# Performance work log

Measured on AMD Instinct MI355X. Metric: run time of the kernel, lower is better.

The kernel has to match this reference:

```python
import jax, jax.numpy as jnp
import numpy as np

ZC, ZS = 32, 16
NS = [16384, 4096, 1024, 256, 64]  # mesh node counts per level
K_CH = 6
DEG = 12

def _key(i):
    return jax.random.fold_in(jax.random.key(0), i)

def setup_inputs():
    d = {}
    d["x"] = jax.random.normal(_key(0), (2, 16, NS[0], 3), jnp.float32)
    enc_dims = [(6, 16), (16, 16), (16, 16), (16, 32)]
    dec_dims = [(32, 16), (16, 16), (16, 16), (16, 3)]
    i = 1
    for p, dims in (("enc", enc_dims), ("decc", dec_dims), ("decs", dec_dims)):
        for l, (fi, fo) in enumerate(dims):
            d[p + "_W" + str(l)] = 0.1 * jax.random.normal(_key(i), (K_CH, fi, fo), jnp.float32); i += 1
            if p == "enc" or l < 3:  # last decoder convs have bias=None
                d[p + "_b" + str(l)] = jnp.zeros((fo,), jnp.float32)
    nfz = NS[4] * 32  # _n_features_before_z
    d["mu_W"] = 0.1 * jax.random.normal(_key(i), (ZC + ZS, nfz), jnp.float32); i += 1
    d["mu_b"] = jnp.zeros((ZC + ZS,), jnp.float32)
    d["linc_W"] = 0.1 * jax.random.normal(_key(i), (nfz, ZC), jnp.float32); i += 1
    d["linc_b"] = jnp.zeros((nfz,), jnp.float32)
    d["lins_W"] = 0.1 * jax.random.normal(_key(i), (nfz, ZC + 2 * ZS), jnp.float32); i += 1
    d["lins_b"] = jnp.zeros((nfz,), jnp.float32)
    for l in range(4):
        d["ei" + str(l)] = jax.random.randint(_key(i), (2, DEG * NS[l]), 0, NS[l], jnp.int32); i += 1
    d["ei4"] = jax.random.randint(_key(i), (2, DEG * NS[0]), 0, NS[0], jnp.int32); i += 1
    for l in range(4):
        d["ds_i" + str(l)] = jax.random.randint(_key(i), (NS[l + 1], 3), 0, NS[l], jnp.int32); i += 1
        d["ds_w" + str(l)] = jax.random.uniform(_key(i), (NS[l + 1], 3), jnp.float32); i += 1
        d["us_i" + str(l)] = jax.random.randint(_key(i), (NS[l], 3), 0, NS[l + 1], jnp.int32); i += 1
        d["us_w" + str(l)] = jax.random.uniform(_key(i), (NS[l], 3), jnp.float32); i += 1
    return d

def _norm(ei, n):
    # ChebConv_Coma.norm: D^-1/2 A D^-1/2 edge weights (unit edge weights)
    row, col = ei[0], ei[1]
    deg = jnp.zeros((n,), jnp.float32).at[row].add(1.0)
    dis = jnp.where(deg > 0, 1.0 / jnp.sqrt(jnp.maximum(deg, 1.0)), 0.0)
    return dis[row] * dis[col]

def _prop(x, ei, w, n):
    # sparse matvec: out[:, dst] += w_e * x[:, src]   (x: [B, n, F])
    msg = x[:, ei[0], :] * w[None, :, None]
    return jnp.zeros((x.shape[0], n, x.shape[2]), x.dtype).at[:, ei[1], :].add(msg)

def _cheb(x, ei, w, Wk, b, n):
    # Chebyshev recurrence: T0=x, T1=Lx, Tk=2L T_{k-1} - T_{k-2}
    out = jnp.einsum('bnf,fg->bng', x, Wk[0])
    Tx0 = x
    Tx1 = _prop(x, ei, w, n)
    out = out + jnp.einsum('bnf,fg->bng', Tx1, Wk[1])
    for k in range(2, Wk.shape[0]):
        Tx2 = 2.0 * _prop(Tx1, ei, w, n) - Tx0
        out = out + jnp.einsum('bnf,fg->bng', Tx2, Wk[k])
        Tx0, Tx1 = Tx1, Tx2
    return out if b is None else out + b

def _pool(x, idx, w):
    # sparse pooling matrix, 3 nnz/row: out[:, i] = sum_k w[i,k] * x[:, idx[i,k]]
    return jnp.einsum('bnkf,nk->bnf', x[:, idx, :], w)

def _phase(x):
    # PhaseTensor: doubles last dim with cos/sin phase modulation over time axis 1
    T = x.shape[1]
    th = 2.0 * jnp.pi * jnp.arange(T, dtype=x.dtype) / T
    shp = (1, T) + (1,) * (x.ndim - 2)
    return jnp.concatenate([x * jnp.cos(th).reshape(shp), x * jnp.sin(th).reshape(shp)], axis=-1)

def _model(FL, IL):
    (x, eW0, eb0, eW1, eb1, eW2, eb2, eW3, eb3,
     cW0, cb0, cW1, cb1, cW2, cb2, cW3,
     sW0, sb0, sW1, sb1, sW2, sb2, sW3,
     mu_W, mu_b, linc_W, linc_b, lins_W, lins_b,
     ds_w0, ds_w1, ds_w2, ds_w3, us_w0, us_w1, us_w2, us_w3) = FL
    (ei0, ei1, ei2, ei3, ei4,
     ds_i0, ds_i1, ds_i2, ds_i3, us_i0, us_i1, us_i2, us_i3) = IL
    eis = [ei0, ei1, ei2, ei3, ei4]
    lvl_n = [NS[0], NS[1], NS[2], NS[3], NS[0]]
    nrm = [_norm(eis[l], lvl_n[l]) for l in range(5)]
    B, T, N0, F0 = x.shape
    # phase_input: [B,T,N,3] -> [B,T,N,6]; fold time into batch for the conv stack
    h = _phase(x).reshape(B * T, N0, 2 * F0)
    encW = [(eW0, eb0), (eW1, eb1), (eW2, eb2), (eW3, eb3)]
    dsl = [(ds_i0, ds_w0), (ds_i1, ds_w1), (ds_i2, ds_w2), (ds_i3, ds_w3)]
    usl = [(us_i0, us_w0), (us_i1, us_w1), (us_i2, us_w2), (us_i3, us_w3)]
    for l in range(4):
        h = jax.nn.relu(_cheb(h, eis[l], nrm[l], encW[l][0], encW[l][1], NS[l]))
        h = _pool(h, dsl[l][0], dsl[l][1])
    h = h.reshape(B, T, -1)  # [B, T, N4*32]
    mu = jnp.einsum('btf,zf->btz', h, mu_W) + mu_b
    # faithful to torch code: per-t cat along dim 0 (time-major) then reshape(-1, T, z)
    mu_c = jnp.mean(jnp.swapaxes(mu[..., :ZC], 0, 1).reshape(B, T, ZC), axis=1)
    mu_s = jnp.mean(jnp.swapaxes(mu[..., ZC:], 0, 1).reshape(B, T, ZS), axis=1)

    def dec(z, Ws, bs, lW, lb, relu_first):
        y = z @ lW.T + lb
        if relu_first:
            y = jax.nn.relu(y)
        y = y.reshape(y.shape[0], NS[4], Ws[0].shape[1])  # [*, N4, 32]
        for i in range(3):  # n_layers - 1 upsample+conv+relu
            lvl = 3 - i
            y = _pool(y, usl[lvl][0], usl[lvl][1])
            y = jax.nn.relu(_cheb(y, eis[lvl], nrm[lvl], Ws[i], bs[i], NS[lvl]))
        y = _pool(y, usl[0][0], usl[0][1])
        return _cheb(y, eis[4], nrm[4], Ws[3], None, NS[0])  # final conv, no bias/relu

    s_avg = dec(mu_c, [cW0, cW1, cW2, cW3], [cb0, cb1, cb2], linc_W, linc_b, False)
    # decoder_s, vectorized over timeframes by folding T into batch
    zs_ph = _phase(jnp.broadcast_to(mu_s[:, None, :], (B, T, ZS)))  # [B,T,2*ZS]
    zc_rep = jnp.broadcast_to(mu_c[:, None, :], (B, T, ZC))
    zin = jnp.concatenate([zc_rep, zs_ph], axis=-1).reshape(B * T, ZC + 2 * ZS)
    ds_t = dec(zin, [sW0, sW1, sW2, sW3], [sb0, sb1, sb2], lins_W, lins_b, True).reshape(B, T, N0, 3)
    s_t = s_avg[:, None] + ds_t
    return mu_c, mu_s, s_avg, s_t

def reference(x, enc_W0, enc_b0, enc_W1, enc_b1, enc_W2, enc_b2, enc_W3, enc_b3, decc_W0, decc_b0, decc_W1, decc_b1, decc_W2, decc_b2, decc_W3, decs_W0, decs_b0, decs_W1, decs_b1, decs_W2, decs_b2, decs_W3, mu_W, mu_b, linc_W, linc_b, lins_W, lins_b, ds_w0, ds_w1, ds_w2, ds_w3, us_w0, us_w1, us_w2, us_w3, ei0, ei1, ei2, ei3, ei4, ds_i0, ds_i1, ds_i2, ds_i3, us_i0, us_i1, us_i2, us_i3):
    FL = (x, enc_W0, enc_b0, enc_W1, enc_b1, enc_W2, enc_b2, enc_W3, enc_b3,
          decc_W0, decc_b0, decc_W1, decc_b1, decc_W2, decc_b2, decc_W3,
          decs_W0, decs_b0, decs_W1, decs_b1, decs_W2, decs_b2, decs_W3,
          mu_W, mu_b, linc_W, linc_b, lins_W, lins_b,
          ds_w0, ds_w1, ds_w2, ds_w3, us_w0, us_w1, us_w2, us_w3)
    IL = (ei0, ei1, ei2, ei3, ei4, ds_i0, ds_i1, ds_i2, ds_i3, us_i0, us_i1, us_i2, us_i3)
    return _model(FL, IL)
```

## Files before the change

kernel.cpp:

```cpp
#include <hip/hip_runtime.h>
#include <cstdint>
#include <cstddef>

#define TPB 256

typedef float f32x4 __attribute__((ext_vector_type(4)));
typedef float f32x2 __attribute__((ext_vector_type(2)));
typedef int   i32x4 __attribute__((ext_vector_type(4)));

static inline int cdiv(long long a, int b){ return (int)((a + (long long)b - 1) / b); }

#define NTOT 38144
#define ETOT 457728
#define CTOT 762880
#define RPTOT 38149


template<int W>
__device__ __forceinline__ void vload(const float* __restrict__ p, float* r){
  if constexpr (W == 8){ vload<4>(p, r); vload<4>(p+4, r+4); }
  else if constexpr (W == 4){ f32x4 v = *reinterpret_cast<const f32x4*>(p); r[0]=v.x;r[1]=v.y;r[2]=v.z;r[3]=v.w; }
  else { f32x2 v = *reinterpret_cast<const f32x2*>(p); r[0]=v.x;r[1]=v.y; }
}
template<int W>
__device__ __forceinline__ void vstore(float* __restrict__ p, const float* r){
  if constexpr (W == 8){ vstore<4>(p, r); vstore<4>(p+4, r+4); }
  else if constexpr (W == 4){ f32x4 v; v.x=r[0];v.y=r[1];v.z=r[2];v.w=r[3]; *reinterpret_cast<f32x4*>(p) = v; }
  else { f32x2 v; v.x=r[0];v.y=r[1]; *reinterpret_cast<f32x2*>(p) = v; }
}

template<int F>
__device__ __forceinline__ void loadrow(const float* __restrict__ p, float* r){
  #pragma unroll
  for (int q = 0; q < F/4; ++q) vload<4>(p + 4*q, r + 4*q);
}
template<int F>
__device__ __forceinline__ void storerow(float* __restrict__ p, const float* r){
  #pragma unroll
  for (int q = 0; q < F/4; ++q) vstore<4>(p + 4*q, r + 4*q);
}


__device__ __forceinline__ bool lvl_edge(int t, const int* e0,const int* e1,const int* e2,const int* e3,const int* e4,
                                         const int*& ei, int& E, int& noff, int& rpoff, int& rel){
  if (t < 196608){ ei=e0; E=196608; noff=0;     rpoff=0;     rel=t;        return true; }
  if (t < 245760){ ei=e1; E=49152;  noff=16384; rpoff=16385; rel=t-196608; return true; }
  if (t < 258048){ ei=e2; E=12288;  noff=20480; rpoff=20482; rel=t-245760; return true; }
  if (t < 261120){ ei=e3; E=3072;   noff=21504; rpoff=21507; rel=t-258048; return true; }
  if (t < 457728){ ei=e4; E=196608; noff=21760; rpoff=21764; rel=t-261120; return true; }
  return false;
}

__global__ void k_degs_all(const int* e0,const int* e1,const int* e2,const int* e3,const int* e4,
                           int* __restrict__ rowdeg, int* __restrict__ dstdeg){
  int t = blockIdx.x*blockDim.x + threadIdx.x;
  const int* ei; int E, noff, rpoff, rel;
  if (!lvl_edge(t, e0,e1,e2,e3,e4, ei,E,noff,rpoff,rel)) return;
  atomicAdd(&rowdeg[noff + ei[rel]], 1);
  atomicAdd(&dstdeg[noff + ei[E + rel]], 1);
}

__global__ void k_dis_all(const int* __restrict__ rowdeg, float* __restrict__ dis){
  int t = blockIdx.x*blockDim.x + threadIdx.x;
  if (t >= NTOT) return;
  int d = rowdeg[t];
  dis[t] = d > 0 ? rsqrtf((float)d) : 0.f;
}

__global__ void k_scan5(const int* __restrict__ dstdeg, int* __restrict__ rp, int* __restrict__ cursor){
  const int NnA[5]  = {16384,4096,1024,256,16384};
  const int NOFF[5] = {0,16384,20480,21504,21760};
  const int COFF[5] = {0,327680,409600,430080,435200};
  __shared__ int part[257];
  int l = blockIdx.x;
  int N = NnA[l];
  const int* cnt = dstdeg + NOFF[l];
  int* rpl = rp + NOFF[l] + l;
  int* cul = cursor + NOFF[l] + l;
  int tid = threadIdx.x;
  int chunk = (N + 255) / 256;
  int lo = tid*chunk; if (lo > N) lo = N;
  int hi = lo + chunk; if (hi > N) hi = N;
  int s = 0;
  for (int i = lo; i < hi; ++i) s += (cnt[i] + 7) & ~7;
  part[tid+1] = s;
  if (tid == 0) part[0] = COFF[l];
  __syncthreads();
  if (tid == 0){ for (int i = 1; i <= 256; ++i) part[i] += part[i-1]; }
  __syncthreads();
  int run = part[tid];
  for (int i = lo; i < hi; ++i){ rpl[i] = run; cul[i] = run; run += (cnt[i] + 7) & ~7; }
  if (tid == 0) rpl[N] = part[256];
}

__global__ void k_fill_all(const int* e0,const int* e1,const int* e2,const int* e3,const int* e4,
                           const float* __restrict__ dis, int* __restrict__ cursor,
                           int* __restrict__ srcs, float* __restrict__ w){
  int t = blockIdx.x*blockDim.x + threadIdx.x;
  const int* ei; int E, noff, rpoff, rel;
  if (!lvl_edge(t, e0,e1,e2,e3,e4, ei,E,noff,rpoff,rel)) return;
  int src = ei[rel], dst = ei[E + rel];
  int pos = atomicAdd(&cursor[rpoff + dst], 1);
  srcs[pos] = src;
  w[pos] = dis[noff + src] * dis[noff + dst];
}

__global__ void k_pad_all(const int* __restrict__ dstdeg, const int* __restrict__ rp,
                          int* __restrict__ srcs, float* __restrict__ w){
  int t = blockIdx.x*blockDim.x + threadIdx.x;
  if (t >= NTOT) return;
  int rpoff, n;
  if      (t < 16384){ rpoff = 0;     n = t; }
  else if (t < 20480){ rpoff = 16385; n = t - 16384; }
  else if (t < 21504){ rpoff = 20482; n = t - 20480; }
  else if (t < 21760){ rpoff = 21507; n = t - 21504; }
  else               { rpoff = 21764; n = t - 21760; }
  int j0 = rp[rpoff + n];
  int j1 = rp[rpoff + n + 1];
  int cnt = dstdeg[t];
  int sfill = cnt > 0 ? srcs[j0] : 0;
  for (int j = j0 + cnt; j < j1; ++j){ srcs[j] = sfill; w[j] = 0.f; }
}


template<int FinPad>
__device__ __forceinline__ void tmap(int N, int& gb, int& n, int& gs, int& sub, int& laneoff){
  constexpr int LPR = FinPad/4;
  gb = blockIdx.x & 7;
  int I = (blockIdx.x >> 3)*256 + threadIdx.x;
  n = I / FinPad;
  int u = I - n*FinPad;
  gs = u / LPR;
  sub = u - gs*LPR;
  laneoff = gs*FinPad + sub*4;
}

template<int FinPad>
__device__ __forceinline__ void gather8_t(const float* __restrict__ base,
                                          const int* __restrict__ srcs, const float* __restrict__ w,
                                          int j0, int j1, int laneoff, float* acc){
  constexpr int RS = 4*FinPad;
  #pragma unroll
  for (int q = 0; q < 4; ++q) acc[q] = 0.f;
  for (int j = j0; j < j1; j += 8){
    i32x4 sa = *reinterpret_cast<const i32x4*>(srcs + j);
    i32x4 sb = *reinterpret_cast<const i32x4*>(srcs + j + 4);
    f32x4 wa = *reinterpret_cast<const f32x4*>(w + j);
    f32x4 wb = *reinterpret_cast<const f32x4*>(w + j + 4);
    float v0[4], v1[4], v2[4], v3[4], v4[4], v5[4], v6[4], v7[4];
    vload<4>(base + (size_t)sa.x*RS + laneoff, v0);
    vload<4>(base + (size_t)sa.y*RS + laneoff, v1);
    vload<4>(base + (size_t)sa.z*RS + laneoff, v2);
    vload<4>(base + (size_t)sa.w*RS + laneoff, v3);
    vload<4>(base + (size_t)sb.x*RS + laneoff, v4);
    vload<4>(base + (size_t)sb.y*RS + laneoff, v5);
    vload<4>(base + (size_t)sb.z*RS + laneoff, v6);
    vload<4>(base + (size_t)sb.w*RS + laneoff, v7);
    #pragma unroll
    for (int q = 0; q < 4; ++q){
      acc[q] = fmaf(wa.x, v0[q], acc[q]);
      acc[q] = fmaf(wa.y, v1[q], acc[q]);
      acc[q] = fmaf(wa.z, v2[q], acc[q]);
      acc[q] = fmaf(wa.w, v3[q], acc[q]);
      acc[q] = fmaf(wb.x, v4[q], acc[q]);
      acc[q] = fmaf(wb.y, v5[q], acc[q]);
      acc[q] = fmaf(wb.z, v6[q], acc[q]);
      acc[q] = fmaf(wb.w, v7[q], acc[q]);
    }
  }
}

template<int FinPad, int FinReal, int Fout>
__device__ __forceinline__ void gemm_t(const float* ts, const float* __restrict__ Wk,
                                       int sub, float* o){
  constexpr int LPR = FinPad/4;
  int lane = (int)threadIdx.x & 63;
  int lanebase = lane & ~(LPR-1);
  float tv[FinPad];
  #pragma unroll
  for (int s = 0; s < LPR; ++s)
    #pragma unroll
    for (int q = 0; q < 4; ++q)
      tv[s*4+q] = __shfl(ts[q], lanebase + s, 64);
  if constexpr (Fout % 4 == 0){
    constexpr int OPL = Fout/LPR;
    #pragma unroll
    for (int fi = 0; fi < FinReal; ++fi)
      #pragma unroll
      for (int q = 0; q < OPL; ++q)
        o[q] = fmaf(tv[fi], Wk[fi*Fout + sub*OPL + q], o[q]);
  } else {
    if (sub < Fout){
      #pragma unroll
      for (int fi = 0; fi < FinReal; ++fi)
        o[0] = fmaf(tv[fi], Wk[fi*Fout + sub], o[0]);
    }
  }
}

template<int FinPad, int PRE>
__global__ void k_pre_t(const float* __restrict__ psrc, const int* __restrict__ pidx,
                        const float* __restrict__ pw, float* __restrict__ bufX,
                        int N, int Nin){
  int gb, n, gs, sub, laneoff;
  tmap<FinPad>(N, gb, n, gs, sub, laneoff);
  constexpr int RS = 4*FinPad;
  float r[4];
  if constexpr (PRE == 1){
    int g = (gb<<2) | gs;
    int t = g & 15;
    float th = 6.283185307179586f * (float)t / 16.0f;
    float sn, cs; sincosf(th, &sn, &cs);
    const float* xr = psrc + ((size_t)g*16384 + n)*3;
    #pragma unroll
    for (int q = 0; q < 4; ++q){
      int f = sub*4 + q;
      float v = 0.f;
      if (f < 6) v = xr[f % 3] * (f < 3 ? cs : sn);
      r[q] = v;
    }
  } else {
    int i0 = pidx[n*3+0], i1 = pidx[n*3+1], i2 = pidx[n*3+2];
    float w0 = pw[n*3+0], w1 = pw[n*3+1], w2 = pw[n*3+2];
    const float* pb = psrc + (size_t)gb*Nin*RS + laneoff;
    float a[4], b[4], c[4];
    vload<4>(pb + (size_t)i0*RS, a);
    vload<4>(pb + (size_t)i1*RS, b);
    vload<4>(pb + (size_t)i2*RS, c);
    #pragma unroll
    for (int q = 0; q < 4; ++q) r[q] = fmaf(w0, a[q], fmaf(w1, b[q], w2*c[q]));
  }
  vstore<4>(bufX + (size_t)gb*N*RS + (size_t)n*RS + laneoff, r);
}

template<int FinPad, int FinReal, int Fout>
__global__ void k_first_t(const int* __restrict__ rp, const int* __restrict__ srcs, const float* __restrict__ w,
                          const float* __restrict__ bufX, float* __restrict__ bufT1, float* __restrict__ out,
                          const float* __restrict__ W6, const float* __restrict__ bias, int N){
  constexpr int LPR = FinPad/4;
  constexpr int OPL = (Fout % 4 == 0) ? Fout/LPR : 1;
  constexpr int RS = 4*FinPad;
  int gb, n, gs, sub, laneoff;
  tmap<FinPad>(N, gb, n, gs, sub, laneoff);
  const float* gbase = bufX + (size_t)gb*N*RS;
  float t0[4]; vload<4>(gbase + (size_t)n*RS + laneoff, t0);
  float t1[4];
  gather8_t<FinPad>(gbase, srcs, w, rp[n], rp[n+1], laneoff, t1);
  vstore<4>(bufT1 + (size_t)gb*N*RS + (size_t)n*RS + laneoff, t1);
  float o[OPL];
  if constexpr (Fout % 4 == 0){
    #pragma unroll
    for (int q = 0; q < OPL; ++q) o[q] = bias ? bias[sub*OPL + q] : 0.f;
  } else {
    o[0] = (bias && sub < Fout) ? bias[sub] : 0.f;
  }
  gemm_t<FinPad,FinReal,Fout>(t0, W6, sub, o);
  gemm_t<FinPad,FinReal,Fout>(t1, W6 + (size_t)FinReal*Fout, sub, o);
  if constexpr (Fout % 4 == 0){
    vstore<OPL>(out + ((size_t)(gb*N + n)*4 + gs)*Fout + sub*OPL, o);
  } else {
    if (sub < Fout){
      int g = (gb<<2)|gs;
      out[((size_t)g*N + n)*3 + sub] = o[0];
    }
  }
}

template<int FinPad, int FinReal, int Fout>
__global__ void k_step_t(const int* __restrict__ rp, const int* __restrict__ srcs, const float* __restrict__ w,
                         const float* __restrict__ Tm1, float* __restrict__ P, float* __restrict__ out,
                         const float* __restrict__ Wk, const float* __restrict__ savg,
                         int N, int relu, int last){
  constexpr int LPR = FinPad/4;
  constexpr int OPL = (Fout % 4 == 0) ? Fout/LPR : 1;
  constexpr int RS = 4*FinPad;
  int gb, n, gs, sub, laneoff;
  tmap<FinPad>(N, gb, n, gs, sub, laneoff);
  const float* gbase = Tm1 + (size_t)gb*N*RS;
  float tk[4];
  gather8_t<FinPad>(gbase, srcs, w, rp[n], rp[n+1], laneoff, tk);
  float tm2[4]; vload<4>(P + (size_t)gb*N*RS + (size_t)n*RS + laneoff, tm2);
  #pragma unroll
  for (int q = 0; q < 4; ++q) tk[q] = 2.f*tk[q] - tm2[q];
  if (!last) vstore<4>(P + (size_t)gb*N*RS + (size_t)n*RS + laneoff, tk);
  float o[OPL];
  if constexpr (Fout % 4 == 0){
    vload<OPL>(out + ((size_t)(gb*N + n)*4 + gs)*Fout + sub*OPL, o);
  } else {
    o[0] = 0.f;
    if (sub < Fout) o[0] = out[((size_t)((gb<<2)|gs)*N + n)*3 + sub];
  }
  gemm_t<FinPad,FinReal,Fout>(tk, Wk, sub, o);
  if constexpr (Fout % 4 == 0){
    if (last && relu){
      #pragma unroll
      for (int q = 0; q < OPL; ++q) o[q] = fmaxf(o[q], 0.f);
    }
    vstore<OPL>(out + ((size_t)(gb*N + n)*4 + gs)*Fout + sub*OPL, o);
  } else {
    if (sub < Fout){
      float v = o[0];
      if (last && relu) v = fmaxf(v, 0.f);
      int g = (gb<<2)|gs;
      if (last && savg) v += savg[((size_t)(g>>4)*N + n)*3 + sub];
      out[((size_t)g*N + n)*3 + sub] = v;
    }
  }
}


template<int FPL, int FinPad>
__device__ __forceinline__ void gather8(const float* __restrict__ gb,
                                        const int* __restrict__ srcs, const float* __restrict__ w,
                                        int j0, int j1, int sub, float* acc){
  #pragma unroll
  for (int q = 0; q < FPL; ++q) acc[q] = 0.f;
  for (int j = j0; j < j1; j += 8){
    i32x4 sa = *reinterpret_cast<const i32x4*>(srcs + j);
    i32x4 sb = *reinterpret_cast<const i32x4*>(srcs + j + 4);
    f32x4 wa = *reinterpret_cast<const f32x4*>(w + j);
    f32x4 wb = *reinterpret_cast<const f32x4*>(w + j + 4);
    float v0[FPL], v1[FPL], v2[FPL], v3[FPL], v4[FPL], v5[FPL], v6[FPL], v7[FPL];
    vload<FPL>(gb + (size_t)sa.x*FinPad + sub*FPL, v0);
    vload<FPL>(gb + (size_t)sa.y*FinPad + sub*FPL, v1);
    vload<FPL>(gb + (size_t)sa.z*FinPad + sub*FPL, v2);
    vload<FPL>(gb + (size_t)sa.w*FinPad + sub*FPL, v3);
    vload<FPL>(gb + (size_t)sb.x*FinPad + sub*FPL, v4);
    vload<FPL>(gb + (size_t)sb.y*FinPad + sub*FPL, v5);
    vload<FPL>(gb + (size_t)sb.z*FinPad + sub*FPL, v6);
    vload<FPL>(gb + (size_t)sb.w*FinPad + sub*FPL, v7);
    #pragma unroll
    for (int q = 0; q < FPL; ++q){
      acc[q] = fmaf(wa.x, v0[q], acc[q]);
      acc[q] = fmaf(wa.y, v1[q], acc[q]);
      acc[q] = fmaf(wa.z, v2[q], acc[q]);
      acc[q] = fmaf(wa.w, v3[q], acc[q]);
      acc[q] = fmaf(wb.x, v4[q], acc[q]);
      acc[q] = fmaf(wb.y, v5[q], acc[q]);
      acc[q] = fmaf(wb.z, v6[q], acc[q]);
      acc[q] = fmaf(wb.w, v7[q], acc[q]);
    }
  }
}

template<int FinPad, int FinReal, int Fout>
__device__ __forceinline__ void gemm_acc(const float* ts, const float* __restrict__ Wk,
                                         int sub, int lanebase, float* o){
  constexpr int FPL = FinPad/4;
  float tv[FinPad];
  #pragma unroll
  for (int s = 0; s < 4; ++s)
    #pragma unroll
    for (int q = 0; q < FPL; ++q)
      tv[s*FPL+q] = __shfl(ts[q], lanebase + s, 64);
  if constexpr (Fout % 4 == 0){
    constexpr int OPL = Fout/4;
    #pragma unroll
    for (int fi = 0; fi < FinReal; ++fi)
      #pragma unroll
      for (int q = 0; q < OPL; ++q)
        o[q] = fmaf(tv[fi], Wk[fi*Fout + sub*OPL + q], o[q]);
  } else {
    if (sub < Fout){
      #pragma unroll
      for (int fi = 0; fi < FinReal; ++fi)
        o[0] = fmaf(tv[fi], Wk[fi*Fout + sub], o[0]);
    }
  }
}

template<int FinPad>
__device__ __forceinline__ void pool_row(const float* __restrict__ psrc, const int* __restrict__ pidx,
                                         const float* __restrict__ pw, int n, int g, int Nin, int sub,
                                         float* r){
  constexpr int FPL = FinPad/4;
  int i0 = pidx[n*3+0], i1 = pidx[n*3+1], i2 = pidx[n*3+2];
  float w0 = pw[n*3+0], w1 = pw[n*3+1], w2 = pw[n*3+2];
  const float* bsrc = psrc + (size_t)g*Nin*FinPad + sub*FPL;
  float a[FPL], b[FPL], c[FPL];
  vload<FPL>(bsrc + (size_t)i0*FinPad, a);
  vload<FPL>(bsrc + (size_t)i1*FinPad, b);
  vload<FPL>(bsrc + (size_t)i2*FinPad, c);
  #pragma unroll
  for (int q = 0; q < FPL; ++q) r[q] = fmaf(w0, a[q], fmaf(w1, b[q], w2*c[q]));
}

template<int FinPad>
__global__ void k_pre_f(const float* __restrict__ psrc, const int* __restrict__ pidx,
                        const float* __restrict__ pw, float* __restrict__ bufX,
                        int G, int logN, int Nin){
  constexpr int FPL = FinPad/4;
  long long i4 = (long long)blockIdx.x*blockDim.x + threadIdx.x;
  if (i4 >= ((long long)G << logN)*4) return;
  int sub = (int)(i4 & 3);
  long long i = i4 >> 2;
  int N = 1 << logN;
  int n = (int)(i & (N-1));
  int g = (int)(i >> logN);
  float r[FPL];
  pool_row<FinPad>(psrc, pidx, pw, n, g, Nin, sub, r);
  vstore<FPL>(bufX + (size_t)i*FinPad + sub*FPL, r);
}

template<int FinPad, int FinReal, int Fout>
__global__ void k_first_f(const int* __restrict__ rp, const int* __restrict__ srcs, const float* __restrict__ w,
                          const float* __restrict__ bufX, float* __restrict__ bufT1, float* __restrict__ out,
                          const float* __restrict__ W6, const float* __restrict__ bias,
                          int G, int logN){
  constexpr int FPL = FinPad/4;
  constexpr int OPL = (Fout % 4 == 0) ? Fout/4 : 1;
  long long i4 = (long long)blockIdx.x*blockDim.x + threadIdx.x;
  if (i4 >= ((long long)G << logN)*4) return;
  int sub = (int)(i4 & 3);
  long long i = i4 >> 2;
  int N = 1 << logN;
  int n = (int)(i & (N-1));
  int lanebase = ((int)threadIdx.x & 63) & ~3;
  const float* gb = bufX + (size_t)(i - n)*FinPad;
  float t0[FPL]; vload<FPL>(bufX + (size_t)i*FinPad + sub*FPL, t0);
  float t1[FPL];
  gather8<FPL,FinPad>(gb, srcs, w, rp[n], rp[n+1], sub, t1);
  vstore<FPL>(bufT1 + (size_t)i*FinPad + sub*FPL, t1);
  float o[OPL];
  if constexpr (Fout % 4 == 0){
    #pragma unroll
    for (int q = 0; q < OPL; ++q) o[q] = bias ? bias[sub*OPL + q] : 0.f;
  } else {
    o[0] = (bias && sub < Fout) ? bias[sub] : 0.f;
  }
  gemm_acc<FinPad,FinReal,Fout>(t0, W6, sub, lanebase, o);
  gemm_acc<FinPad,FinReal,Fout>(t1, W6 + (size_t)FinReal*Fout, sub, lanebase, o);
  if constexpr (Fout % 4 == 0) vstore<OPL>(out + (size_t)i*Fout + sub*OPL, o);
  else if (sub < Fout) out[(size_t)i*Fout + sub] = o[0];
}

template<int FinPad, int FinReal, int Fout>
__global__ void k_step_f(const int* __restrict__ rp, const int* __restrict__ srcs, const float* __restrict__ w,
                         const float* __restrict__ Tm1, float* __restrict__ P, float* __restrict__ out,
                         const float* __restrict__ Wk, const float* __restrict__ savg,
                         int G, int logN, int relu, int last){
  constexpr int FPL = FinPad/4;
  constexpr int OPL = (Fout % 4 == 0) ? Fout/4 : 1;
  long long i4 = (long long)blockIdx.x*blockDim.x + threadIdx.x;
  if (i4 >= ((long long)G << logN)*4) return;
  int sub = (int)(i4 & 3);
  long long i = i4 >> 2;
  int N = 1 << logN;
  int n = (int)(i & (N-1));
  int lanebase = ((int)threadIdx.x & 63) & ~3;
  const float* gb = Tm1 + (size_t)(i - n)*FinPad;
  float tk[FPL];
  gather8<FPL,FinPad>(gb, srcs, w, rp[n], rp[n+1], sub, tk);
  float tm2[FPL]; vload<FPL>(P + (size_t)i*FinPad + sub*FPL, tm2);
  #pragma unroll
  for (int q = 0; q < FPL; ++q) tk[q] = 2.f*tk[q] - tm2[q];
  if (!last) vstore<FPL>(P + (size_t)i*FinPad + sub*FPL, tk);
  float o[OPL];
  if constexpr (Fout % 4 == 0) vload<OPL>(out + (size_t)i*Fout + sub*OPL, o);
  else { o[0] = (sub < Fout) ? out[(size_t)i*Fout + sub] : 0.f; }
  gemm_acc<FinPad,FinReal,Fout>(tk, Wk, sub, lanebase, o);
  if constexpr (Fout % 4 == 0){
    if (last && relu){
      #pragma unroll
      for (int q = 0; q < OPL; ++q) o[q] = fmaxf(o[q], 0.f);
    }
    vstore<OPL>(out + (size_t)i*Fout + sub*OPL, o);
  } else {
    if (sub < Fout){
      float v = o[0];
      if (last && relu) v = fmaxf(v, 0.f);
      if (last && savg){
        int g = (int)(i >> logN);
        v += savg[((size_t)(g>>4)*N + n)*3 + sub];
      }
      out[(size_t)i*Fout + sub] = v;
    }
  }
}


__global__ void k_mu_t(const float* __restrict__ h_t, const float* __restrict__ W,
                       const float* __restrict__ b, float* __restrict__ mu){
  int wid = (blockIdx.x*blockDim.x + threadIdx.x) >> 6;
  int lane = threadIdx.x & 63;
  if (wid >= 32*48) return;
  int z = wid % 48, g = wid / 48;
  const float* wr = W + (size_t)z*2048;
  const float* hb = h_t + (size_t)(g>>2)*64*128 + (g&3)*32;
  float acc = 0.f;
  for (int f2 = lane; f2 < 2048; f2 += 64)
    acc = fmaf(hb[(size_t)(f2>>5)*128 + (f2&31)], wr[f2], acc);
  for (int o = 32; o > 0; o >>= 1) acc += __shfl_down(acc, o, 64);
  if (lane == 0) mu[wid] = acc + b[z];
}

__global__ void k_mucs(const float* __restrict__ mu, float* __restrict__ muc,
                       float* __restrict__ mus, float* __restrict__ out){
  int i = blockIdx.x*blockDim.x + threadIdx.x;
  if (i >= 96) return;
  int z = i % 48, bp = i / 48;
  float acc = 0.f;
  for (int b = 0; b < 2; ++b)
    for (int t = 8*bp; t < 8*bp + 8; ++t)
      acc += mu[(b*16 + t)*48 + z];
  acc *= (1.f/16.f);
  if (z < 32){ muc[bp*32 + z] = acc; out[bp*32 + z] = acc; }
  else       { mus[bp*16 + (z-32)] = acc; out[64 + bp*16 + (z-32)] = acc; }
}

__global__ void k_zin(const float* __restrict__ muc, const float* __restrict__ mus,
                      float* __restrict__ zin){
  int i = blockIdx.x*blockDim.x + threadIdx.x;
  if (i >= 32*64) return;
  int c = i % 64, g = i / 64;
  int b = g / 16, t = g % 16;
  float v;
  if (c < 32){
    v = muc[b*32 + c];
  } else {
    float th = 6.283185307179586f * (float)t / 16.0f;
    int k = c - 32;
    int kk = (k < 16) ? k : (k - 16);
    float m = mus[b*16 + kk];
    v = (k < 16) ? m * cosf(th) : m * sinf(th);
  }
  zin[i] = v;
}

__global__ void k_lin(const float* __restrict__ z, const float* __restrict__ W,
                      const float* __restrict__ b, float* __restrict__ y,
                      int G, int Z, int relu){
  int i = blockIdx.x*blockDim.x + threadIdx.x;
  if (i >= G*2048) return;
  int f = i % 2048, g = i / 2048;
  const float* zr = z + (size_t)g*Z;
  const float* wr = W + (size_t)f*Z;
  float acc = b[f];
  for (int k = 0; k < Z; ++k) acc = fmaf(zr[k], wr[k], acc);
  if (relu) acc = fmaxf(acc, 0.f);
  y[i] = acc;
}

__global__ void k_lin_t(const float* __restrict__ z, const float* __restrict__ W,
                        const float* __restrict__ b, float* __restrict__ y_t,
                        int Z, int relu){
  int i = blockIdx.x*blockDim.x + threadIdx.x;
  if (i >= 32*2048) return;
  int f2 = i % 2048, g = i / 2048;
  const float* zr = z + (size_t)g*Z;
  const float* wr = W + (size_t)f2*Z;
  float acc = b[f2];
  for (int k = 0; k < Z; ++k) acc = fmaf(zr[k], wr[k], acc);
  if (relu) acc = fmaxf(acc, 0.f);
  y_t[(size_t)(g>>2)*64*128 + (size_t)(f2>>5)*128 + (g&3)*32 + (f2&31)] = acc;
}


struct LvlArgs {
  const int* rp; const int* srcs; const float* w;
  const float* psrc; const int* pidx; const float* pw;
  float* bufX; float* bufT1; float* out;
  const float* W6; const float* bias; const float* savg;
  int G; int logN; int Nin; int relu;
};

template<int FinPad, int FinReal, int Fout, int PRE>
static void run_level_t(hipStream_t s, const LvlArgs& a){
  int N = 1 << a.logN;
  int grid = 8 * (N*FinPad/256);
  k_pre_t<FinPad,PRE><<<grid,256,0,s>>>(a.psrc, a.pidx, a.pw, a.bufX, N, a.Nin);
  k_first_t<FinPad,FinReal,Fout><<<grid,256,0,s>>>(a.rp, a.srcs, a.w, a.bufX, a.bufT1, a.out,
                                                   a.W6, a.bias, N);
  float* Ab = a.bufT1; float* Bb = a.bufX;
  for (int k = 2; k <= 5; ++k){
    int last = (k == 5) ? 1 : 0;
    k_step_t<FinPad,FinReal,Fout><<<grid,256,0,s>>>(a.rp, a.srcs, a.w, Ab, Bb, a.out,
                                                    a.W6 + (size_t)k*FinReal*Fout,
                                                    last ? a.savg : nullptr,
                                                    N, a.relu, last);
    float* t = Ab; Ab = Bb; Bb = t;
  }
}

template<int FinPad, int FinReal, int Fout>
static void run_level_f(hipStream_t s, const LvlArgs& a){
  long long GN4 = ((long long)a.G << a.logN) * 4;
  int grid = cdiv(GN4, 256);
  k_pre_f<FinPad><<<grid,256,0,s>>>(a.psrc, a.pidx, a.pw, a.bufX, a.G, a.logN, a.Nin);
  k_first_f<FinPad,FinReal,Fout><<<grid,256,0,s>>>(a.rp, a.srcs, a.w, a.bufX, a.bufT1, a.out,
                                                   a.W6, a.bias, a.G, a.logN);
  float* Ab = a.bufT1; float* Bb = a.bufX;
  for (int k = 2; k <= 5; ++k){
    int last = (k == 5) ? 1 : 0;
    k_step_f<FinPad,FinReal,Fout><<<grid,256,0,s>>>(a.rp, a.srcs, a.w, Ab, Bb, a.out,
                                                    a.W6 + (size_t)k*FinReal*Fout,
                                                    last ? a.savg : nullptr,
                                                    a.G, a.logN, a.relu, last);
    float* t = Ab; Ab = Bb; Bb = t;
  }
}

extern "C" void kernel_launch(void* const* d_in, const int* in_sizes, int n_in,
                              void* d_out, int out_size, void* d_ws, size_t ws_size,
                              hipStream_t stream){
  const float* x = (const float*)d_in[0];
  const float* encW[4] = {(const float*)d_in[1],(const float*)d_in[3],(const float*)d_in[5],(const float*)d_in[7]};
  const float* encB[4] = {(const float*)d_in[2],(const float*)d_in[4],(const float*)d_in[6],(const float*)d_in[8]};
  const float* ccW[4]  = {(const float*)d_in[9],(const float*)d_in[11],(const float*)d_in[13],(const float*)d_in[15]};
  const float* ccB[3]  = {(const float*)d_in[10],(const float*)d_in[12],(const float*)d_in[14]};
  const float* csW[4]  = {(const float*)d_in[16],(const float*)d_in[18],(const float*)d_in[20],(const float*)d_in[22]};
  const float* csB[3]  = {(const float*)d_in[17],(const float*)d_in[19],(const float*)d_in[21]};
  const float* muW  = (const float*)d_in[23]; const float* muB  = (const float*)d_in[24];
  const float* lincW = (const float*)d_in[25]; const float* lincB = (const float*)d_in[26];
  const float* linsW = (const float*)d_in[27]; const float* linsB = (const float*)d_in[28];
  const int* ei[5] = {(const int*)d_in[29],(const int*)d_in[30],(const int*)d_in[31],
                      (const int*)d_in[32],(const int*)d_in[33]};
  const int* ds_i[4]; const float* ds_w[4]; const int* us_i[4]; const float* us_w[4];
  for (int l = 0; l < 4; ++l){
    ds_i[l] = (const int*)d_in[34 + 4*l]; ds_w[l] = (const float*)d_in[35 + 4*l];
    us_i[l] = (const int*)d_in[36 + 4*l]; us_w[l] = (const float*)d_in[37 + 4*l];
  }

  float* ws = (float*)d_ws;
  const size_t BIG = 8388608;
  float* B0 = ws + 0*BIG;
  float* B1 = ws + 1*BIG;
  float* B2 = ws + 2*BIG;
  float* B3 = ws + 3*BIG;
  size_t off = 4*BIG;

  int*   rp_all     = (int*)(ws + off); off += RPTOT;
  int*   cursor_all = (int*)(ws + off); off += RPTOT;
  off = (off + 3) & ~(size_t)3;
  int*   srcs_all   = (int*)(ws + off); off += CTOT;
  float* w_all      =        ws + off;  off += CTOT;
  int*   rowdeg     = (int*)(ws + off); off += NTOT;
  int*   dstdeg     = (int*)(ws + off); off += NTOT;
  float* dis        =        ws + off;  off += NTOT;
  float* hmu        =        ws + off;  off += (size_t)32*2048;
  float* mu         =        ws + off;  off += (size_t)32*48;
  float* muc        =        ws + off;  off += 64;
  float* mus        =        ws + off;  off += 32;
  float* zin        =        ws + off;  off += (size_t)32*64;

  float* outp = (float*)d_out;
  float* out_savg = outp + 96;
  float* out_st   = outp + 96 + 98304;

  hipMemsetAsync(rowdeg, 0, 2*(size_t)NTOT*sizeof(int), stream);
  k_degs_all<<<cdiv(ETOT,TPB),TPB,0,stream>>>(ei[0],ei[1],ei[2],ei[3],ei[4], rowdeg, dstdeg);
  k_dis_all<<<cdiv(NTOT,TPB),TPB,0,stream>>>(rowdeg, dis);
  k_scan5<<<5,256,0,stream>>>(dstdeg, rp_all, cursor_all);
  k_fill_all<<<cdiv(ETOT,TPB),TPB,0,stream>>>(ei[0],ei[1],ei[2],ei[3],ei[4], dis, cursor_all, srcs_all, w_all);
  k_pad_all<<<cdiv(NTOT,TPB),TPB,0,stream>>>(dstdeg, rp_all, srcs_all, w_all);

  const int RPOFF[5] = {0,16385,20482,21507,21764};
  const int* RP[5];
  for (int l = 0; l < 5; ++l) RP[l] = rp_all + RPOFF[l];

  run_level_t<8,6,16,1>(stream, {RP[0],srcs_all,w_all, x,nullptr,nullptr,
                                 B0,B1,B2, encW[0],encB[0],nullptr, 32,14,0,1});
  run_level_t<16,16,16,0>(stream, {RP[1],srcs_all,w_all, B2,ds_i[0],ds_w[0],
                                   B0,B1,B3, encW[1],encB[1],nullptr, 32,12,16384,1});
  run_level_t<16,16,16,0>(stream, {RP[2],srcs_all,w_all, B3,ds_i[1],ds_w[1],
                                   B0,B1,B2, encW[2],encB[2],nullptr, 32,10,4096,1});
  run_level_t<16,16,32,0>(stream, {RP[3],srcs_all,w_all, B2,ds_i[2],ds_w[2],
                                   B0,B1,B3, encW[3],encB[3],nullptr, 32,8,1024,1});
  {
    int grid = 8 * (64*32/256);
    k_pre_t<32,0><<<grid,256,0,stream>>>(B3, ds_i[3], ds_w[3], hmu, 64, 256);
  }

  k_mu_t<<<cdiv((long long)32*48*64,TPB),TPB,0,stream>>>(hmu, muW, muB, mu);
  k_mucs<<<1,128,0,stream>>>(mu, muc, mus, outp);

  k_lin<<<cdiv((long long)2*2048,TPB),TPB,0,stream>>>(muc, lincW, lincB, B2, 2, 32, 0);
  run_level_f<32,32,16>(stream, {RP[3],srcs_all,w_all, B2,us_i[3],us_w[3],
                                 B0,B1,B3, ccW[0],ccB[0],nullptr, 2,8,64,1});
  run_level_f<16,16,16>(stream, {RP[2],srcs_all,w_all, B3,us_i[2],us_w[2],
                                 B0,B1,B2, ccW[1],ccB[1],nullptr, 2,10,256,1});
  run_level_f<16,16,16>(stream, {RP[1],srcs_all,w_all, B2,us_i[1],us_w[1],
                                 B0,B1,B3, ccW[2],ccB[2],nullptr, 2,12,1024,1});
  run_level_f<16,16,3>(stream, {RP[4],srcs_all,w_all, B3,us_i[0],us_w[0],
                                B0,B1,out_savg, ccW[3],nullptr,nullptr, 2,14,4096,0});

  k_zin<<<cdiv(32*64,TPB),TPB,0,stream>>>(muc, mus, zin);
  k_lin_t<<<cdiv((long long)32*2048,TPB),TPB,0,stream>>>(zin, linsW, linsB, B2, 64, 1);
  run_level_t<32,32,16,0>(stream, {RP[3],srcs_all,w_all, B2,us_i[3],us_w[3],
                                   B0,B1,B3, csW[0],csB[0],nullptr, 32,8,64,1});
  run_level_t<16,16,16,0>(stream, {RP[2],srcs_all,w_all, B3,us_i[2],us_w[2],
                                   B0,B1,B2, csW[1],csB[1],nullptr, 32,10,256,1});
  run_level_t<16,16,16,0>(stream, {RP[1],srcs_all,w_all, B2,us_i[1],us_w[1],
                                   B0,B1,B3, csW[2],csB[2],nullptr, 32,12,1024,1});
  run_level_t<16,16,3,0>(stream, {RP[4],srcs_all,w_all, B3,us_i[0],us_w[0],
                                  B0,B1,out_st, csW[3],nullptr,out_savg, 32,14,4096,0});

  (void)in_sizes; (void)n_in; (void)out_size; (void)ws_size;
}
```

Measured before the change: 1.103 ms.

## Overlap content decoder and first pre-pass with main path on side stream

Creates a second non-blocking stream with events. The first-level input pre-pass runs concurrently with CSR graph construction, and the content decoder (2-graph batch) runs concurrently with the style decoder using separate scratch buffers D0-D3. The main stream waits on events only before the final style level, which needs out_savg. This targets the serialization of small, under-occupied kernels, at the cost of extra workspace and event synchronisation overhead.

```diff
diff --git a/kernel.cpp b/kernel.cpp
--- a/kernel.cpp
+++ b/kernel.cpp
@@ -14,6 +14,18 @@
 #define ETOT 457728
 #define CTOT 762880
 #define RPTOT 38149
+
+static hipStream_t g_s2 = nullptr;
+static hipEvent_t g_evF1 = nullptr, g_evPre = nullptr, g_evF2 = nullptr, g_evDecc = nullptr;
+__attribute__((constructor)) static void init_side_stream(){
+  if (hipStreamCreateWithFlags(&g_s2, hipStreamNonBlocking) != hipSuccess){ g_s2 = nullptr; return; }
+  if (hipEventCreateWithFlags(&g_evF1, hipEventDisableTiming) != hipSuccess ||
+      hipEventCreateWithFlags(&g_evPre, hipEventDisableTiming) != hipSuccess ||
+      hipEventCreateWithFlags(&g_evF2, hipEventDisableTiming) != hipSuccess ||
+      hipEventCreateWithFlags(&g_evDecc, hipEventDisableTiming) != hipSuccess){
+    g_s2 = nullptr;
+  }
+}
 
 
 template<int W>
@@ -370,22 +382,6 @@
 }
 
 template<int FinPad>
-__device__ __forceinline__ void pool_row(const float* __restrict__ psrc, const int* __restrict__ pidx,
-                                         const float* __restrict__ pw, int n, int g, int Nin, int sub,
-                                         float* r){
-  constexpr int FPL = FinPad/4;
-  int i0 = pidx[n*3+0], i1 = pidx[n*3+1], i2 = pidx[n*3+2];
-  float w0 = pw[n*3+0], w1 = pw[n*3+1], w2 = pw[n*3+2];
-  const float* bsrc = psrc + (size_t)g*Nin*FinPad + sub*FPL;
-  float a[FPL], b[FPL], c[FPL];
-  vload<FPL>(bsrc + (size_t)i0*FinPad, a);
-  vload<FPL>(bsrc + (size_t)i1*FinPad, b);
-  vload<FPL>(bsrc + (size_t)i2*FinPad, c);
-  #pragma unroll
-  for (int q = 0; q < FPL; ++q) r[q] = fmaf(w0, a[q], fmaf(w1, b[q], w2*c[q]));
-}
-
-template<int FinPad>
 __global__ void k_pre_f(const float* __restrict__ psrc, const int* __restrict__ pidx,
                         const float* __restrict__ pw, float* __restrict__ bufX,
                         int G, int logN, int Nin){
@@ -397,8 +393,15 @@
   int N = 1 << logN;
   int n = (int)(i & (N-1));
   int g = (int)(i >> logN);
-  float r[FPL];
-  pool_row<FinPad>(psrc, pidx, pw, n, g, Nin, sub, r);
+  int i0 = pidx[n*3+0], i1 = pidx[n*3+1], i2 = pidx[n*3+2];
+  float w0 = pw[n*3+0], w1 = pw[n*3+1], w2 = pw[n*3+2];
+  const float* bsrc = psrc + (size_t)g*Nin*FinPad + sub*FPL;
+  float a[FPL], b[FPL], c[FPL], r[FPL];
+  vload<FPL>(bsrc + (size_t)i0*FinPad, a);
+  vload<FPL>(bsrc + (size_t)i1*FinPad, b);
+  vload<FPL>(bsrc + (size_t)i2*FinPad, c);
+  #pragma unroll
+  for (int q = 0; q < FPL; ++q) r[q] = fmaf(w0, a[q], fmaf(w1, b[q], w2*c[q]));
   vstore<FPL>(bufX + (size_t)i*FinPad + sub*FPL, r);
 }
 
@@ -565,10 +568,11 @@
 };
 
 template<int FinPad, int FinReal, int Fout, int PRE>
-static void run_level_t(hipStream_t s, const LvlArgs& a){
+static void run_level_t(hipStream_t s, const LvlArgs& a, bool do_pre = true){
   int N = 1 << a.logN;
   int grid = 8 * (N*FinPad/256);
-  k_pre_t<FinPad,PRE><<<grid,256,0,s>>>(a.psrc, a.pidx, a.pw, a.bufX, N, a.Nin);
+  if (do_pre)
+    k_pre_t<FinPad,PRE><<<grid,256,0,s>>>(a.psrc, a.pidx, a.pw, a.bufX, N, a.Nin);
   k_first_t<FinPad,FinReal,Fout><<<grid,256,0,s>>>(a.rp, a.srcs, a.w, a.bufX, a.bufT1, a.out,
                                                    a.W6, a.bias, N);
   float* Ab = a.bufT1; float* Bb = a.bufX;
@@ -642,10 +646,29 @@
   float* muc        =        ws + off;  off += 64;
   float* mus        =        ws + off;  off += 32;
   float* zin        =        ws + off;  off += (size_t)32*64;
+  const size_t DSM = (size_t)2*16384*16;
+  float* D0 = ws + off; off += DSM;
+  float* D1 = ws + off; off += DSM;
+  float* D2 = ws + off; off += DSM;
+  float* D3 = ws + off; off += DSM;
 
   float* outp = (float*)d_out;
   float* out_savg = outp + 96;
   float* out_st   = outp + 96 + 98304;
+
+  const bool use2 = (g_s2 != nullptr);
+  hipStream_t sC = use2 ? g_s2 : stream;
+
+  if (use2){
+    hipEventRecord(g_evF1, stream);
+    hipStreamWaitEvent(g_s2, g_evF1, 0);
+  }
+  {
+    int N = 16384;
+    int grid = 8 * (N*8/256);
+    k_pre_t<8,1><<<grid,256,0,sC>>>(x, nullptr, nullptr, B0, N, 0);
+    if (use2) hipEventRecord(g_evPre, g_s2);
+  }
 
   hipMemsetAsync(rowdeg, 0, 2*(size_t)NTOT*sizeof(int), stream);
   k_degs_all<<<cdiv(ETOT,TPB),TPB,0,stream>>>(ei[0],ei[1],ei[2],ei[3],ei[4], rowdeg, dstdeg);
@@ -653,13 +676,14 @@
   k_scan5<<<5,256,0,stream>>>(dstdeg, rp_all, cursor_all);
   k_fill_all<<<cdiv(ETOT,TPB),TPB,0,stream>>>(ei[0],ei[1],ei[2],ei[3],ei[4], dis, cursor_all, srcs_all, w_all);
   k_pad_all<<<cdiv(NTOT,TPB),TPB,0,stream>>>(dstdeg, rp_all, srcs_all, w_all);
+  if (use2) hipStreamWaitEvent(stream, g_evPre, 0);
 
   const int RPOFF[5] = {0,16385,20482,21507,21764};
   const int* RP[5];
   for (int l = 0; l < 5; ++l) RP[l] = rp_all + RPOFF[l];
 
   run_level_t<8,6,16,1>(stream, {RP[0],srcs_all,w_all, x,nullptr,nullptr,
-                                 B0,B1,B2, encW[0],encB[0],nullptr, 32,14,0,1});
+                                 B0,B1,B2, encW[0],encB[0],nullptr, 32,14,0,1}, false);
   run_level_t<16,16,16,0>(stream, {RP[1],srcs_all,w_all, B2,ds_i[0],ds_w[0],
                                    B0,B1,B3, encW[1],encB[1],nullptr, 32,12,16384,1});
   run_level_t<16,16,16,0>(stream, {RP[2],srcs_all,w_all, B3,ds_i[1],ds_w[1],
@@ -674,15 +698,20 @@
   k_mu_t<<<cdiv((long long)32*48*64,TPB),TPB,0,stream>>>(hmu, muW, muB, mu);
   k_mucs<<<1,128,0,stream>>>(mu, muc, mus, outp);
 
-  k_lin<<<cdiv((long long)2*2048,TPB),TPB,0,stream>>>(muc, lincW, lincB, B2, 2, 32, 0);
-  run_level_f<32,32,16>(stream, {RP[3],srcs_all,w_all, B2,us_i[3],us_w[3],
-                                 B0,B1,B3, ccW[0],ccB[0],nullptr, 2,8,64,1});
-  run_level_f<16,16,16>(stream, {RP[2],srcs_all,w_all, B3,us_i[2],us_w[2],
-                                 B0,B1,B2, ccW[1],ccB[1],nullptr, 2,10,256,1});
-  run_level_f<16,16,16>(stream, {RP[1],srcs_all,w_all, B2,us_i[1],us_w[1],
-                                 B0,B1,B3, ccW[2],ccB[2],nullptr, 2,12,1024,1});
-  run_level_f<16,16,3>(stream, {RP[4],srcs_all,w_all, B3,us_i[0],us_w[0],
-                                B0,B1,out_savg, ccW[3],nullptr,nullptr, 2,14,4096,0});
+  if (use2){
+    hipEventRecord(g_evF2, stream);
+    hipStreamWaitEvent(g_s2, g_evF2, 0);
+  }
+  k_lin<<<cdiv((long long)2*2048,TPB),TPB,0,sC>>>(muc, lincW, lincB, D2, 2, 32, 0);
+  run_level_f<32,32,16>(sC, {RP[3],srcs_all,w_all, D2,us_i[3],us_w[3],
+                             D0,D1,D3, ccW[0],ccB[0],nullptr, 2,8,64,1});
+  run_level_f<16,16,16>(sC, {RP[2],srcs_all,w_all, D3,us_i[2],us_w[2],
+                             D0,D1,D2, ccW[1],ccB[1],nullptr, 2,10,256,1});
+  run_level_f<16,16,16>(sC, {RP[1],srcs_all,w_all, D2,us_i[1],us_w[1],
+                             D0,D1,D3, ccW[2],ccB[2],nullptr, 2,12,1024,1});
+  run_level_f<16,16,3>(sC, {RP[4],srcs_all,w_all, D3,us_i[0],us_w[0],
+                            D0,D1,out_savg, ccW[3],nullptr,nullptr, 2,14,4096,0});
+  if (use2) hipEventRecord(g_evDecc, g_s2);
 
   k_zin<<<cdiv(32*64,TPB),TPB,0,stream>>>(muc, mus, zin);
   k_lin_t<<<cdiv((long long)32*2048,TPB),TPB,0,stream>>>(zin, linsW, linsB, B2, 64, 1);
@@ -692,6 +721,7 @@
                                    B0,B1,B2, csW[1],csB[1],nullptr, 32,10,256,1});
   run_level_t<16,16,16,0>(stream, {RP[1],srcs_all,w_all, B2,us_i[1],us_w[1],
                                    B0,B1,B3, csW[2],csB[2],nullptr, 32,12,1024,1});
+  if (use2) hipStreamWaitEvent(stream, g_evDecc, 0);
   run_level_t<16,16,3,0>(stream, {RP[4],srcs_all,w_all, B3,us_i[0],us_w[0],
                                   B0,B1,out_st, csW[3],nullptr,out_savg, 32,14,4096,0});
 
```

After: 1.125 ms. No clear change (+1.9%).
